# Kernel tuning notes

Measured on AMD Instinct MI355X. Metric: run time of the kernel, lower is better.

## Reference

```python
import jax, jax.numpy as jnp
import numpy as np

B, T, F, H, FC = 32, 2048, 128, 512, 128


def setup_inputs() -> dict:
    key = jax.random.key(0)
    ks = jax.random.split(key, 10)
    x = jax.random.normal(ks[0], (B, T, F), dtype=jnp.float32)
    lengths = jax.random.randint(ks[1], (B,), 1, T + 1)
    s = 1.0 / np.sqrt(H)  # torch nn.RNN init: U(-1/sqrt(hidden), 1/sqrt(hidden))
    W_ih = jax.random.uniform(ks[2], (H, F), jnp.float32, -s, s)
    W_hh = jax.random.uniform(ks[3], (H, H), jnp.float32, -s, s)
    b_ih = jax.random.uniform(ks[4], (H,), jnp.float32, -s, s)
    b_hh = jax.random.uniform(ks[5], (H,), jnp.float32, -s, s)
    s1 = 1.0 / np.sqrt(H)
    W1 = jax.random.uniform(ks[6], (FC, H), jnp.float32, -s1, s1)
    b1 = jax.random.uniform(ks[7], (FC,), jnp.float32, -s1, s1)
    s2 = 1.0 / np.sqrt(FC)
    W2 = jax.random.uniform(ks[8], (1, FC), jnp.float32, -s2, s2)
    b2 = jax.random.uniform(ks[9], (1,), jnp.float32, -s2, s2)
    return {"x": x, "lengths": lengths, "W_ih": W_ih, "W_hh": W_hh,
            "b_ih": b_ih, "b_hh": b_hh, "W1": W1, "b1": b1, "W2": W2, "b2": b2}


def reference(x, lengths, W_ih, W_hh, b_ih, b_hh, W1, b1, W2, b2):
    # x: [B, T, F] padded ragged sequences; lengths: [B]
    Bs, Ts, Fs = x.shape
    Hs = W_ih.shape[0]
    mask = jnp.arange(Ts)[None, :] < lengths[:, None]          # [B, T]
    xs = (jnp.swapaxes(x, 0, 1), mask.T)                       # time-major [T, B, ...]

    def step(h, inp):
        x_t, m_t = inp
        # vanilla RNN cell: h' = tanh(W_ih x + b_ih + W_hh h + b_hh)
        h_new = jnp.tanh(x_t @ W_ih.T + b_ih + h @ W_hh.T + b_hh)
        h = jnp.where(m_t[:, None], h_new, h)                  # freeze hidden past seq end
        return h, h_new

    h0 = jnp.zeros((Bs, Hs), dtype=x.dtype)
    h_final, outp = jax.lax.scan(step, h0, xs)                 # h_final [B,H], outp [T,B,H]

    # fcn: Linear(H,128) -> Linear(128,1) -> ReLU, applied to every timestep output
    n = jax.nn.relu((outp @ W1.T + b1) @ W2.T + b2)            # [T, B, 1]
    pos = (n[..., 0] > 0) & mask.T                             # count only valid timesteps
    outs = jnp.sum(pos, axis=0).astype(jnp.float32)[:, None]   # [B, 1]
    return outs, h_final
```

## Files before the change

### kernel.cpp

```cpp
#include <hip/hip_runtime.h>
#include <math.h>
#include <stdint.h>

#define BB 32
#define TT 2048
#define FF 128
#define HH 512
#define FCC 128
#define QW 8
#define NTH 640

#define SCALE_F     1073741824.0f
#define INV_SCALE_F (1.0f/1073741824.0f)
#define CNT_ONE     (1ull<<48)
#define LOW_MASK    ((1ull<<48)-1ull)
#define BIAS_TOTAL  (1ll<<46)
#define BIAS_SHARE  (1ll<<43)

typedef float f32x2 __attribute__((ext_vector_type(2)));

__global__ void ws_zero(uint64_t* g) {
    g[(size_t)blockIdx.x * blockDim.x + threadIdx.x] = 0ull;
}

__device__ __forceinline__ void wait_lgkm0() {
    asm volatile("s_waitcnt lgkmcnt(0)" ::: "memory");
}

__device__ __forceinline__ float fast_tanh(float z) {
    float ax = fabsf(z);
    float e  = __expf(-2.0f * ax);
    float r  = (1.0f - e) / (1.0f + e);
    return copysignf(r, z);
}

__device__ __forceinline__ void pk_fma(f32x2& d, f32x2 a, f32x2 b) {
    asm("v_pk_fma_f32 %0, %1, %2, %0" : "+v"(d) : "v"(a), "v"(b));
}
__device__ __forceinline__ f32x2 lo2(float4 v) { f32x2 r; r.x = v.x; r.y = v.y; return r; }
__device__ __forceinline__ f32x2 hi2(float4 v) { f32x2 r; r.x = v.z; r.y = v.w; return r; }

__global__ __launch_bounds__(NTH, 1)
void rnn_seq(const float* __restrict__ x, const int* __restrict__ lengths,
             const float* __restrict__ W_ih, const float* __restrict__ W_hh,
             const float* __restrict__ b_ih, const float* __restrict__ b_hh,
             const float* __restrict__ W1, const float* __restrict__ b1,
             const float* __restrict__ W2, const float* __restrict__ b2,
             float* __restrict__ out, uint64_t* __restrict__ ws)
{
    const int blk  = blockIdx.x;
    const int b    = blk >> 3;
    const int q    = blk & 7;
    const int tid  = threadIdx.x;
    const int w    = tid >> 6;
    const int lane = tid & 63;
    const int len  = lengths[b];

    uint64_t* gh  = ws;
    uint64_t* gsd = ws + 2 * BB * HH;

    __shared__ float hsh[2][64];
    __shared__ float biass[64];
    __shared__ int   flag_s;

    if (w == 8) {
        biass[lane] = b_ih[q * 64 + lane] + b_hh[q * 64 + lane];
        hsh[0][lane] = 0.0f;
        if (lane == 0) flag_s = 0;
    }
    __syncthreads();

    if (w < 8) {
        const int r = w * 64 + lane;
        float4 ww[16];
        { const float4* p = (const float4*)(W_hh + (size_t)r * HH + q * 64);
          #pragma unroll
          for (int k = 0; k < 16; ++k) ww[k] = p[k]; }
        float4 wi[4];
        { const float4* p = (const float4*)(W_ih + r * FF + q * 16);
          #pragma unroll
          for (int k = 0; k < 4; ++k) wi[k] = p[k]; }
        float wvreg = 0.0f;
        if (w == 7) {
            const int col = q * 64 + lane;
            #pragma unroll 8
            for (int f = 0; f < FCC; ++f) wvreg += W2[f] * W1[f * HH + col];
        }
        long long prevA[2] = {0, 0};
        const float* xb = x + (size_t)b * TT * FF + q * 16;
        float4 xc[4], xn[4];
        { const float4* p = (const float4*)xb;
          #pragma unroll
          for (int k = 0; k < 4; ++k) xc[k] = p[k]; }
        { const float4* p = (const float4*)(xb + FF);
          #pragma unroll
          for (int k = 0; k < 4; ++k) xn[k] = p[k]; }

        uint64_t* ghb = gh + (size_t)b * HH + r;

        for (int i = 0; i < len; ++i) {
            f32x2 acc01 = {0.0f, 0.0f};
            f32x2 acc23 = {0.0f, 0.0f};
            #pragma unroll
            for (int k = 0; k < 4; ++k) {
                pk_fma(acc01, lo2(wi[k]), lo2(xc[k]));
                pk_fma(acc23, hi2(wi[k]), hi2(xc[k]));
            }

            while (__hip_atomic_load(&flag_s, __ATOMIC_RELAXED,
                                     __HIP_MEMORY_SCOPE_WORKGROUP) < i) {}
            const float* hc = hsh[i & 1];
            const float4* hq = (const float4*)hc;
            #pragma unroll
            for (int k = 0; k < 16; ++k) {
                float4 hk = hq[k];
                pk_fma(acc01, lo2(ww[k]), lo2(hk));
                pk_fma(acc23, hi2(ww[k]), hi2(hk));
            }
            float A = (acc01.x + acc01.y) + (acc23.x + acc23.y);

            float hown = 0.0f;
            if (w == 7) hown = hc[lane];

            long long f = llrintf(A * SCALE_F);
            const int pn = (i + 1) & 1;
            long long con = (long long)CNT_ONE + (f - prevA[pn])
                          + ((i < 2) ? BIAS_SHARE : 0);
            prevA[pn] = f;
            atomicAdd((unsigned long long*)(ghb + (size_t)pn * BB * HH),
                      (unsigned long long)con);

            if (w == 7 && i > 0) {
                float d = hown * wvreg;
                d += __shfl_xor(d, 1);  d += __shfl_xor(d, 2);
                d += __shfl_xor(d, 4);  d += __shfl_xor(d, 8);
                d += __shfl_xor(d, 16); d += __shfl_xor(d, 32);
                if (lane == 0) {
                    uint64_t pk = ((uint64_t)(uint32_t)i << 32) |
                                  (uint64_t)__float_as_uint(d);
                    __hip_atomic_store(&gsd[((size_t)b * 16 + (i & 15)) * 8 + q],
                                       pk, __ATOMIC_RELAXED, __HIP_MEMORY_SCOPE_AGENT);
                }
            }
            #pragma unroll
            for (int k = 0; k < 4; ++k) xc[k] = xn[k];
            if (i + 2 < len) {
                const float4* p = (const float4*)(xb + (size_t)(i + 2) * FF);
                #pragma unroll
                for (int k = 0; k < 4; ++k) xn[k] = p[k];
            }
        }
        if (w == 7) {
            while (__hip_atomic_load(&flag_s, __ATOMIC_RELAXED,
                                     __HIP_MEMORY_SCOPE_WORKGROUP) < len) {}
            float d = hsh[len & 1][lane] * wvreg;
            d += __shfl_xor(d, 1);  d += __shfl_xor(d, 2);
            d += __shfl_xor(d, 4);  d += __shfl_xor(d, 8);
            d += __shfl_xor(d, 16); d += __shfl_xor(d, 32);
            if (lane == 0) {
                uint64_t pk = ((uint64_t)(uint32_t)len << 32) |
                              (uint64_t)__float_as_uint(d);
                __hip_atomic_store(&gsd[((size_t)b * 16 + (len & 15)) * 8 + q],
                                   pk, __ATOMIC_RELAXED, __HIP_MEMORY_SCOPE_AGENT);
            }
        }
    } else if (w == 8) {
        __builtin_amdgcn_s_setprio(1);
        float hval = 0.0f;
        for (int i = 0; i < len; ++i) {
            const int j  = i + 1;
            const int pn = j & 1;
            const uint64_t target = 8ull * (uint64_t)((j + 1) >> 1);
            uint64_t* pr = gh + (size_t)pn * BB * HH + (size_t)b * HH + q * 64 + lane;
            uint64_t u;
            do { u = __hip_atomic_load(pr, __ATOMIC_RELAXED,
                                       __HIP_MEMORY_SCOPE_AGENT); }
            while ((u >> 48) != target);
            long long sf = (long long)(u & LOW_MASK) - BIAS_TOTAL;
            float pre = (float)sf * INV_SCALE_F + biass[lane];
            hval = fast_tanh(pre);
            hsh[pn][lane] = hval;
            wait_lgkm0();
            if (lane == 0)
                __hip_atomic_store(&flag_s, j, __ATOMIC_RELAXED,
                                   __HIP_MEMORY_SCOPE_WORKGROUP);
        }
        out[BB + b * HH + q * 64 + lane] = hval;
    } else {
        if (q != 0) return;
        float cconst = b2[0];
        for (int f = 0; f < FCC; ++f) cconst += W2[f] * b1[f];
        int count = 0;
        for (int j = 1; j <= len; ++j) {
            float d = 0.0f;
            if (lane < 8) {
                uint64_t* pr = gsd + ((size_t)b * 16 + (j & 15)) * 8 + lane;
                uint64_t u;
                do { u = __hip_atomic_load(pr, __ATOMIC_RELAXED,
                                           __HIP_MEMORY_SCOPE_AGENT); }
                while ((int)(u >> 32) != j);
                d = __uint_as_float((uint32_t)u);
            }
            d += __shfl_xor(d, 1); d += __shfl_xor(d, 2); d += __shfl_xor(d, 4);
            if (lane == 0 && d + cconst > 0.0f) ++count;
        }
        if (lane == 0) out[b] = (float)count;
    }
}

extern "C" void kernel_launch(void* const* d_in, const int* in_sizes, int n_in,
                              void* d_out, int out_size, void* d_ws, size_t ws_size,
                              hipStream_t stream) {
    const float* x    = (const float*)d_in[0];
    const int*   lens = (const int*)d_in[1];
    const float* W_ih = (const float*)d_in[2];
    const float* W_hh = (const float*)d_in[3];
    const float* b_ih = (const float*)d_in[4];
    const float* b_hh = (const float*)d_in[5];
    const float* W1   = (const float*)d_in[6];
    const float* b1   = (const float*)d_in[7];
    const float* W2   = (const float*)d_in[8];
    const float* b2   = (const float*)d_in[9];
    float* out = (float*)d_out;
    uint64_t* ws = (uint64_t*)d_ws;

    ws_zero<<<dim3(144), dim3(256), 0, stream>>>(ws);
    rnn_seq<<<dim3(BB * QW), dim3(NTH), 0, stream>>>(
        x, lens, W_ih, W_hh, b_ih, b_hh, W1, b1, W2, b2, out, ws);
}
```

Baseline: 2.839 ms.

## Pipeline spin-wait polling loads and shrink fixed-point accumulator to 32-bit math

The cross-block and in-block spin waits now keep several agent-scope or workgroup-scope loads in flight at once. The global wait also requires the whole wave to see the target count (`__all`) before leaving. This is meant to cut the latency of each poll round trip on the per-timestep critical path. The fixed-point scale drops from 2^30 to 2^22, so quantized contributions fit in 32-bit ints. Decoding then reads only the low 32 bits, which removes 64-bit convert and mask work but coarsens the hidden-state pre-activation resolution.

Measured after the change: 3.172 ms. 1.12x slower.

```diff
diff --git a/kernel.cpp b/kernel.cpp
--- a/kernel.cpp
+++ b/kernel.cpp
@@ -10,10 +10,9 @@
 #define QW 8
 #define NTH 640
 
-#define SCALE_F     1073741824.0f
-#define INV_SCALE_F (1.0f/1073741824.0f)
+#define SCALE_F     4194304.0f
+#define INV_SCALE_F (1.0f/4194304.0f)
 #define CNT_ONE     (1ull<<48)
-#define LOW_MASK    ((1ull<<48)-1ull)
 #define BIAS_TOTAL  (1ll<<46)
 #define BIAS_SHARE  (1ll<<43)
 
@@ -39,6 +38,13 @@
 }
 __device__ __forceinline__ f32x2 lo2(float4 v) { f32x2 r; r.x = v.x; r.y = v.y; return r; }
 __device__ __forceinline__ f32x2 hi2(float4 v) { f32x2 r; r.x = v.z; r.y = v.w; return r; }
+
+__device__ __forceinline__ uint64_t gld_agent(const uint64_t* p) {
+    return __hip_atomic_load(p, __ATOMIC_RELAXED, __HIP_MEMORY_SCOPE_AGENT);
+}
+__device__ __forceinline__ int flag_ld(const int* p) {
+    return __hip_atomic_load(p, __ATOMIC_RELAXED, __HIP_MEMORY_SCOPE_WORKGROUP);
+}
 
 __global__ __launch_bounds__(NTH, 1)
 void rnn_seq(const float* __restrict__ x, const int* __restrict__ lengths,
@@ -86,7 +92,7 @@
             #pragma unroll 8
             for (int f = 0; f < FCC; ++f) wvreg += W2[f] * W1[f * HH + col];
         }
-        long long prevA[2] = {0, 0};
+        int prevI[2] = {0, 0};
         const float* xb = x + (size_t)b * TT * FF + q * 16;
         float4 xc[4], xn[4];
         { const float4* p = (const float4*)xb;
@@ -107,8 +113,16 @@
                 pk_fma(acc23, hi2(wi[k]), hi2(xc[k]));
             }
 
-            while (__hip_atomic_load(&flag_s, __ATOMIC_RELAXED,
-                                     __HIP_MEMORY_SCOPE_WORKGROUP) < i) {}
+            {
+                int f0 = flag_ld(&flag_s);
+                int f1 = flag_ld(&flag_s);
+                for (;;) {
+                    if (f0 >= i) break;
+                    f0 = flag_ld(&flag_s);
+                    if (f1 >= i) break;
+                    f1 = flag_ld(&flag_s);
+                }
+            }
             const float* hc = hsh[i & 1];
             const float4* hq = (const float4*)hc;
             #pragma unroll
@@ -122,11 +136,11 @@
             float hown = 0.0f;
             if (w == 7) hown = hc[lane];
 
-            long long f = llrintf(A * SCALE_F);
+            int fi = __float2int_rn(A * SCALE_F);
             const int pn = (i + 1) & 1;
-            long long con = (long long)CNT_ONE + (f - prevA[pn])
+            long long con = (long long)CNT_ONE + (long long)(fi - prevI[pn])
                           + ((i < 2) ? BIAS_SHARE : 0);
-            prevA[pn] = f;
+            prevI[pn] = fi;
             atomicAdd((unsigned long long*)(ghb + (size_t)pn * BB * HH),
                       (unsigned long long)con);
 
@@ -151,8 +165,7 @@
             }
         }
         if (w == 7) {
-            while (__hip_atomic_load(&flag_s, __ATOMIC_RELAXED,
-                                     __HIP_MEMORY_SCOPE_WORKGROUP) < len) {}
+            while (flag_ld(&flag_s) < len) {}
             float d = hsh[len & 1][lane] * wvreg;
             d += __shfl_xor(d, 1);  d += __shfl_xor(d, 2);
             d += __shfl_xor(d, 4);  d += __shfl_xor(d, 8);
@@ -173,11 +186,21 @@
             const uint64_t target = 8ull * (uint64_t)((j + 1) >> 1);
             uint64_t* pr = gh + (size_t)pn * BB * HH + (size_t)b * HH + q * 64 + lane;
             uint64_t u;
-            do { u = __hip_atomic_load(pr, __ATOMIC_RELAXED,
-                                       __HIP_MEMORY_SCOPE_AGENT); }
-            while ((u >> 48) != target);
-            long long sf = (long long)(u & LOW_MASK) - BIAS_TOTAL;
-            float pre = (float)sf * INV_SCALE_F + biass[lane];
+            uint64_t u0 = gld_agent(pr);
+            uint64_t u1 = gld_agent(pr);
+            uint64_t u2 = gld_agent(pr);
+            uint64_t u3 = gld_agent(pr);
+            for (;;) {
+                if (__all((u0 >> 48) == target)) { u = u0; break; }
+                u0 = gld_agent(pr);
+                if (__all((u1 >> 48) == target)) { u = u1; break; }
+                u1 = gld_agent(pr);
+                if (__all((u2 >> 48) == target)) { u = u2; break; }
+                u2 = gld_agent(pr);
+                if (__all((u3 >> 48) == target)) { u = u3; break; }
+                u3 = gld_agent(pr);
+            }
+            float pre = (float)(int)(uint32_t)u * INV_SCALE_F + biass[lane];
             hval = fast_tanh(pre);
             hsh[pn][lane] = hval;
             wait_lgkm0();
@@ -196,8 +219,7 @@
             if (lane < 8) {
                 uint64_t* pr = gsd + ((size_t)b * 16 + (j & 15)) * 8 + lane;
                 uint64_t u;
-                do { u = __hip_atomic_load(pr, __ATOMIC_RELAXED,
-                                           __HIP_MEMORY_SCOPE_AGENT); }
+                do { u = gld_agent(pr); }
                 while ((int)(u >> 32) != j);
                 d = __uint_as_float((uint32_t)u);
             }
```
